# Optimization experiments

Hardware: AMD Instinct MI355X
Metric: run time of the kernel (lower is better)

## Reference

```python
import jax, jax.numpy as jnp
import numpy as np
import math

B, C, H, W, K, HID = 8, 64, 512, 512, 8, 64

def setup_inputs() -> dict:
    key = jax.random.key(0)
    ks = jax.random.split(key, 12)
    s = 0.05  # weight scale
    return {
        "x": jax.random.normal(ks[0], (B, C, H, W), dtype=jnp.float32),
        "w1k": jax.random.normal(ks[1], (1, HID), dtype=jnp.float32) * s,
        "b1k": jax.random.normal(ks[2], (HID,), dtype=jnp.float32) * s,
        "w2k": jax.random.normal(ks[3], (HID, K * K), dtype=jnp.float32) * s,
        "b2k": jax.random.normal(ks[4], (K * K,), dtype=jnp.float32) * s,
        "w1b": jax.random.normal(ks[5], (1, HID), dtype=jnp.float32) * s,
        "b1b": jax.random.normal(ks[6], (HID,), dtype=jnp.float32) * s,
        "w2b": jax.random.normal(ks[7], (HID, 1), dtype=jnp.float32) * s,
        "b2b": jax.random.normal(ks[8], (1,), dtype=jnp.float32) * s,
        "conv_w": jax.random.normal(ks[9], (C, C), dtype=jnp.float32) * s,
        "conv_b": jax.random.normal(ks[10], (C,), dtype=jnp.float32) * s,
    }

def _patch_pos_dist(h, w, k):
    # normalized distance of each KxK patch center from the image center, row-major over (nh, nw)
    nh, nw = h // k, w // k
    cy, cx = h / 2.0, w / 2.0
    max_d = math.sqrt(cy ** 2 + cx ** 2)
    py = jnp.arange(nh, dtype=jnp.float32) * k + k / 2.0
    px = jnp.arange(nw, dtype=jnp.float32) * k + k / 2.0
    d = jnp.sqrt((py - cy)[:, None] ** 2 + (px - cx)[None, :] ** 2) / max_d
    return d.reshape(nh * nw)  # [L]

def reference(x, w1k, b1k, w2k, b2k, w1b, b1b, w2b, b2b, conv_w, conv_b):
    b, c, h, w = x.shape
    kk = w2k.shape[1]
    k = int(round(math.sqrt(kk)))
    nh, nw = h // k, w // k
    L = nh * nw

    d = _patch_pos_dist(h, w, k)[:, None]  # [L, 1]
    # dynamic per-patch-position kernels and bias (exact-erf GELU as in torch default)
    pk = jax.nn.gelu(d @ w1k + b1k, approximate=False) @ w2k + b2k          # [L, K*K]
    pb = (jax.nn.gelu(d @ w1b + b1b, approximate=False) @ w2b + b2b)[:, 0]  # [L]

    # non-overlapping unfold: [B, C, K*K, L], patches row-major over (nh, nw)
    patches = (x.reshape(b, c, nh, k, nw, k)
                 .transpose(0, 1, 2, 4, 3, 5)
                 .reshape(b, c, L, kk)
                 .transpose(0, 1, 3, 2))

    feats = jnp.einsum('bckl,lk->bcl', patches, pk) + pb[None, None, :]     # [B, C, L]
    feats = jnp.einsum('oc,bcl->bol', conv_w, feats) + conv_b[None, :, None]  # 1x1 conv

    mod = patches * feats[:, :, None, :]  # [B, C, K*K, L]

    # fold back (non-overlapping, so a pure reshape/scatter)
    out = (mod.transpose(0, 1, 3, 2)
              .reshape(b, c, nh, nw, k, k)
              .transpose(0, 1, 2, 4, 3, 5)
              .reshape(b, c, h, w))
    return out
```

## Files before the change

kernel.cpp:

```cpp
#include <hip/hip_runtime.h>
#include <math.h>


static __device__ __forceinline__ float gelu_erf(float x) {
    return 0.5f * x * (1.0f + erff(x * 0.70710678118654752f));
}

__global__ __launch_bounds__(256) void mlp_precompute(
    const float* __restrict__ w1k, const float* __restrict__ b1k,
    const float* __restrict__ w2k, const float* __restrict__ b2k,
    const float* __restrict__ w1b, const float* __restrict__ b1b,
    const float* __restrict__ w2b, const float* __restrict__ b2b,
    float* __restrict__ pk_out,
    float* __restrict__ pb_out)
{
    constexpr int HID = 64;
    const int tid = threadIdx.x;
    const int pi  = tid >> 6;
    const int j   = tid & 63;
    const int l   = blockIdx.x * 4 + pi;

    const int py_i = l >> 6;
    const int px_i = l & 63;
    const float py = (float)(py_i * 8) + 4.0f - 256.0f;
    const float px = (float)(px_i * 8) + 4.0f - 256.0f;
    const float dd = sqrtf(py * py + px * px) * (1.0f / 362.03867196751236f);

    __shared__ float gk[4][HID];
    __shared__ float gb[4][HID];

    gk[pi][j] = gelu_erf(dd * w1k[j] + b1k[j]);
    gb[pi][j] = gelu_erf(dd * w1b[j] + b1b[j]);
    __syncthreads();

    float s = b2k[j];
#pragma unroll 8
    for (int h = 0; h < HID; ++h)
        s += gk[pi][h] * w2k[h * HID + j];
    pk_out[l * HID + j] = s;

    if (j == 0) {
        float t = b2b[0];
        for (int h = 0; h < HID; ++h)
            t += gb[pi][h] * w2b[h];
        pb_out[l] = t;
    }
}

__global__ __launch_bounds__(1024, 4) void afpm_main(
    const float* __restrict__ x,
    const float* __restrict__ conv_w, const float* __restrict__ conv_b,
    const float* __restrict__ pk_g,
    const float* __restrict__ pb_g,
    float* __restrict__ out)
{
    constexpr int W = 512;

    const int tid  = threadIdx.x;
    const int u    = tid & 15;
    const int c    = tid >> 4;
    const int tile = blockIdx.x;
    const int ph   = blockIdx.y;
    const int b    = blockIdx.z;

    __shared__ float pkL[16][68];
    __shared__ float f0T[16][68];
    __shared__ float pbL[16];

    const int lbase = ph * 64 + tile * 16;

    const size_t base = (((size_t)b * 64 + c) * 512 + (size_t)ph * 8) * (size_t)W
                        + (size_t)(tile * 128);
    const float* xp0 = x + base + 4 * u;
    const float* xp1 = x + base + 64 + 4 * u;
    float4 v0[8], v1[8];
#pragma unroll
    for (int r = 0; r < 8; ++r) {
        v0[r] = *(const float4*)(xp0 + r * W);
        v1[r] = *(const float4*)(xp1 + r * W);
    }

    pkL[tid >> 6][tid & 63] = pk_g[(size_t)lbase * 64 + tid];
    if (tid < 16) pbL[tid] = pb_g[lbase + tid];
    __syncthreads();

    const int p0 = u >> 1;
    const int p1 = 8 + (u >> 1);
    const int co = (u & 1) * 4;
    float s0 = 0.0f, s1 = 0.0f;
#pragma unroll
    for (int r = 0; r < 8; ++r) {
        const int k0 = r * 8 + co;
        const float4 a = v0[r];
        s0 += a.x * pkL[p0][k0 + 0] + a.y * pkL[p0][k0 + 1]
            + a.z * pkL[p0][k0 + 2] + a.w * pkL[p0][k0 + 3];
        const float4 d = v1[r];
        s1 += d.x * pkL[p1][k0 + 0] + d.y * pkL[p1][k0 + 1]
            + d.z * pkL[p1][k0 + 2] + d.w * pkL[p1][k0 + 3];
    }
    s0 += __shfl_xor(s0, 1);
    s1 += __shfl_xor(s1, 1);
    if ((u & 1) == 0) f0T[p0][c] = s0 + pbL[p0];
    else              f0T[p1][c] = s1 + pbL[p1];
    __syncthreads();

    float t = 0.0f;
    const float4* cw = (const float4*)(conv_w + (size_t)c * 64);
#pragma unroll
    for (int i = 0; i < 16; ++i) {
        const float4 w = cw[i];
        const float4 f = *(const float4*)&f0T[u][i * 4];
        t += w.x * f.x + w.y * f.y + w.z * f.z + w.w * f.w;
    }
    const float m_self = t + conv_b[c];

    const int lane  = tid & 63;
    const int laneC = lane & 48;
    const float m0 = __shfl(m_self, laneC + p0);
    const float m1 = __shfl(m_self, laneC + p1);

    float* op0 = out + base + 4 * u;
    float* op1 = out + base + 64 + 4 * u;
#pragma unroll
    for (int r = 0; r < 8; ++r) {
        float4 a = v0[r];
        a.x *= m0; a.y *= m0; a.z *= m0; a.w *= m0;
        *(float4*)(op0 + r * W) = a;
        float4 d = v1[r];
        d.x *= m1; d.y *= m1; d.z *= m1; d.w *= m1;
        *(float4*)(op1 + r * W) = d;
    }
}

extern "C" void kernel_launch(void* const* d_in, const int* in_sizes, int n_in,
                              void* d_out, int out_size, void* d_ws, size_t ws_size,
                              hipStream_t stream) {
    const float* x      = (const float*)d_in[0];
    const float* w1k    = (const float*)d_in[1];
    const float* b1k    = (const float*)d_in[2];
    const float* w2k    = (const float*)d_in[3];
    const float* b2k    = (const float*)d_in[4];
    const float* w1b    = (const float*)d_in[5];
    const float* b1b    = (const float*)d_in[6];
    const float* w2b    = (const float*)d_in[7];
    const float* b2b    = (const float*)d_in[8];
    const float* conv_w = (const float*)d_in[9];
    const float* conv_b = (const float*)d_in[10];
    float* out = (float*)d_out;

    constexpr int L = 64 * 64;
    float* pk = (float*)d_ws;
    float* pb = pk + (size_t)L * 64;

    mlp_precompute<<<L / 4, 256, 0, stream>>>(w1k, b1k, w2k, b2k,
                                              w1b, b1b, w2b, b2b, pk, pb);

    dim3 grid(4, 64, 8);
    afpm_main<<<grid, 1024, 0, stream>>>(x, conv_w, conv_b, pk, pb, out);
}
```

Baseline: 226.4 us.

## Map one thread per patch and re-read x instead of holding it in registers

Each thread now owns a whole 8x8 patch for one channel and reads its dynamic kernel directly from global memory, replacing the LDS staging of pk/pb and the lane-pair shuffle reduction. The x tile is no longer kept in 64 registers across the barrier; it is loaded again from global (hopefully from cache) in the output pass. This lowers register pressure enough to raise the launch-bound occupancy hint from 4 to 8. The trade-off is a second read of x, plus row access where each thread covers 32 contiguous bytes and a 16-lane group spans 512 bytes per row, which may coalesce less well.

```diff
diff --git a/kernel.cpp b/kernel.cpp
--- a/kernel.cpp
+++ b/kernel.cpp
@@ -47,7 +47,7 @@
     }
 }
 
-__global__ __launch_bounds__(1024, 4) void afpm_main(
+__global__ __launch_bounds__(1024, 8) void afpm_main(
     const float* __restrict__ x,
     const float* __restrict__ conv_w, const float* __restrict__ conv_b,
     const float* __restrict__ pk_g,
@@ -63,45 +63,26 @@
     const int ph   = blockIdx.y;
     const int b    = blockIdx.z;
 
-    __shared__ float pkL[16][68];
     __shared__ float f0T[16][68];
-    __shared__ float pbL[16];
 
-    const int lbase = ph * 64 + tile * 16;
+    const int l = ph * 64 + tile * 16 + u;
 
     const size_t base = (((size_t)b * 64 + c) * 512 + (size_t)ph * 8) * (size_t)W
                         + (size_t)(tile * 128);
-    const float* xp0 = x + base + 4 * u;
-    const float* xp1 = x + base + 64 + 4 * u;
-    float4 v0[8], v1[8];
+    const float* xp = x + base + u * 8;
+    const float* kp = pk_g + (size_t)l * 64;
+
+    float s = 0.0f;
 #pragma unroll
     for (int r = 0; r < 8; ++r) {
-        v0[r] = *(const float4*)(xp0 + r * W);
-        v1[r] = *(const float4*)(xp1 + r * W);
+        const float4 xa = *(const float4*)(xp + r * W);
+        const float4 xb = *(const float4*)(xp + r * W + 4);
+        const float4 ka = *(const float4*)(kp + r * 8);
+        const float4 kb = *(const float4*)(kp + r * 8 + 4);
+        s += xa.x * ka.x + xa.y * ka.y + xa.z * ka.z + xa.w * ka.w
+           + xb.x * kb.x + xb.y * kb.y + xb.z * kb.z + xb.w * kb.w;
     }
-
-    pkL[tid >> 6][tid & 63] = pk_g[(size_t)lbase * 64 + tid];
-    if (tid < 16) pbL[tid] = pb_g[lbase + tid];
-    __syncthreads();
-
-    const int p0 = u >> 1;
-    const int p1 = 8 + (u >> 1);
-    const int co = (u & 1) * 4;
-    float s0 = 0.0f, s1 = 0.0f;
-#pragma unroll
-    for (int r = 0; r < 8; ++r) {
-        const int k0 = r * 8 + co;
-        const float4 a = v0[r];
-        s0 += a.x * pkL[p0][k0 + 0] + a.y * pkL[p0][k0 + 1]
-            + a.z * pkL[p0][k0 + 2] + a.w * pkL[p0][k0 + 3];
-        const float4 d = v1[r];
-        s1 += d.x * pkL[p1][k0 + 0] + d.y * pkL[p1][k0 + 1]
-            + d.z * pkL[p1][k0 + 2] + d.w * pkL[p1][k0 + 3];
-    }
-    s0 += __shfl_xor(s0, 1);
-    s1 += __shfl_xor(s1, 1);
-    if ((u & 1) == 0) f0T[p0][c] = s0 + pbL[p0];
-    else              f0T[p1][c] = s1 + pbL[p1];
+    f0T[u][c] = s + pb_g[l];
     __syncthreads();
 
     float t = 0.0f;
@@ -112,23 +93,17 @@
         const float4 f = *(const float4*)&f0T[u][i * 4];
         t += w.x * f.x + w.y * f.y + w.z * f.z + w.w * f.w;
     }
-    const float m_self = t + conv_b[c];
+    const float m = t + conv_b[c];
 
-    const int lane  = tid & 63;
-    const int laneC = lane & 48;
-    const float m0 = __shfl(m_self, laneC + p0);
-    const float m1 = __shfl(m_self, laneC + p1);
-
-    float* op0 = out + base + 4 * u;
-    float* op1 = out + base + 64 + 4 * u;
+    float* op = out + base + u * 8;
 #pragma unroll
     for (int r = 0; r < 8; ++r) {
-        float4 a = v0[r];
-        a.x *= m0; a.y *= m0; a.z *= m0; a.w *= m0;
-        *(float4*)(op0 + r * W) = a;
-        float4 d = v1[r];
-        d.x *= m1; d.y *= m1; d.z *= m1; d.w *= m1;
-        *(float4*)(op1 + r * W) = d;
+        float4 xa = *(const float4*)(xp + r * W);
+        float4 xb = *(const float4*)(xp + r * W + 4);
+        xa.x *= m; xa.y *= m; xa.z *= m; xa.w *= m;
+        xb.x *= m; xb.y *= m; xb.z *= m; xb.w *= m;
+        *(float4*)(op + r * W)     = xa;
+        *(float4*)(op + r * W + 4) = xb;
     }
 }
 
```

Result: slower. 561.2 us (+147.9%).
